# Performance work log

Hardware: AMD Instinct MI355X
Metric: run time of the kernel (lower is better)

Reference implementation:

```python
import jax, jax.numpy as jnp
import numpy as np

D, H, W = 20, 18, 18      # f_dim = (20, 72//4, 72//4); depth == feature_ch
PI = 3.14159              # constant used in the torch module


def make_grid():
    # matches make_coordinate_grid_3d: normalized coords in [-1, 1]
    x = 2.0 * jnp.arange(W, dtype=jnp.float32) / (W - 1) - 1.0
    y = 2.0 * jnp.arange(H, dtype=jnp.float32) / (H - 1) - 1.0
    z = 2.0 * jnp.arange(D, dtype=jnp.float32) / (D - 1) - 1.0
    xx = jnp.broadcast_to(x[None, None, :], (D, H, W))
    yy = jnp.broadcast_to(y[None, :, None], (D, H, W))
    zz = jnp.broadcast_to(z[:, None, None], (D, H, W))
    grid_xy = jnp.stack([xx, yy], axis=-1)   # (D,H,W,2), order (x, y)
    return grid_xy, zz


def trilinear_sample(vol, grid):
    # vol: (D,H,W); grid: (D,H,W,3) with (x,y,z) in [-1,1]
    # F.grid_sample defaults: mode='bilinear' (trilinear), padding='zeros', align_corners=False
    ix = ((grid[..., 0] + 1.0) * W - 1.0) * 0.5
    iy = ((grid[..., 1] + 1.0) * H - 1.0) * 0.5
    iz = ((grid[..., 2] + 1.0) * D - 1.0) * 0.5
    x0, y0, z0 = jnp.floor(ix), jnp.floor(iy), jnp.floor(iz)
    wx, wy, wz = ix - x0, iy - y0, iz - z0
    vflat = vol.reshape(-1)
    out = jnp.zeros_like(ix)
    for cz in (0, 1):
        for cy in (0, 1):
            for cx in (0, 1):
                xi = x0 + cx
                yi = y0 + cy
                zi = z0 + cz
                w = ((wx if cx else 1.0 - wx)
                     * (wy if cy else 1.0 - wy)
                     * (wz if cz else 1.0 - wz))
                valid = ((xi >= 0) & (xi < W) & (yi >= 0) & (yi < H)
                         & (zi >= 0) & (zi < D))
                xi_c = jnp.clip(xi, 0, W - 1).astype(jnp.int32)
                yi_c = jnp.clip(yi, 0, H - 1).astype(jnp.int32)
                zi_c = jnp.clip(zi, 0, D - 1).astype(jnp.int32)
                idx = (zi_c * H + yi_c) * W + xi_c
                out = out + jnp.where(valid, w * vflat[idx], 0.0)
    return out


def setup_inputs() -> dict:
    key = jax.random.key(0)
    ks = jax.random.split(key, 10)
    B, P, F = 4096, 256, 20
    s = 0.05
    return {
        "feature_map": jax.random.normal(ks[0], (B, F, H, W), jnp.float32),
        "para_code": jax.random.normal(ks[1], (B, P), jnp.float32),
        "W1": jax.random.normal(ks[2], (P, P), jnp.float32) * s,
        "b1": jax.random.normal(ks[3], (P,), jnp.float32) * s,
        "Ws": jax.random.normal(ks[4], (P, F), jnp.float32) * s,
        "bs": jax.random.normal(ks[5], (F,), jnp.float32) * s,
        "Wr": jax.random.normal(ks[6], (P, F), jnp.float32) * s,
        "br": jax.random.normal(ks[7], (F,), jnp.float32) * s,
        "Wt": jax.random.normal(ks[8], (P, 2 * F), jnp.float32) * s,
        "bt": jax.random.normal(ks[9], (2 * F,), jnp.float32) * s,
    }


def reference(feature_map, para_code, W1, b1, Ws, bs, Wr, br, Wt, bt):
    B, F = feature_map.shape[0], feature_map.shape[1]  # F == D == 20
    grid_xy, grid_z = make_grid()
    h = jax.nn.relu(para_code @ W1 + b1)                     # commn_linear
    scale = jax.nn.sigmoid(h @ Ws + bs) * 2.0                # (B,F)
    angle = jnp.tanh(h @ Wr + br) * PI                       # (B,F)
    trans = jnp.tanh(h @ Wt + bt).reshape(B, F, 2)           # (B,F,2)
    c, s = jnp.cos(angle), jnp.sin(angle)
    rot = jnp.stack([jnp.stack([c, -s], -1),
                     jnp.stack([s, c], -1)], -2)             # (B,F,2,2)
    g = grid_xy.reshape(F, H * W, 2)                          # depth == feature_ch
    # per-channel affine: rotate, scale, translate each grid point
    tg = jnp.einsum('bfij,fpj->bfpi', rot, g)                 # (B,F,HW,2)
    tg = tg * scale[:, :, None, None] + trans[:, :, None, :]
    full_grid = jnp.concatenate(
        [tg.reshape(B, F, H, W, 2),
         jnp.broadcast_to(grid_z, (B, F, H, W))[..., None]], axis=-1)
    return jax.vmap(trilinear_sample)(feature_map, full_grid)
```

## Files before the change

### kernel.cpp

```cpp
#include <hip/hip_runtime.h>

#define PI_F 3.14159f

__global__ __launch_bounds__(256) void params_kernel(
    const float* __restrict__ pc, const float* __restrict__ W1, const float* __restrict__ b1,
    const float* __restrict__ Ws, const float* __restrict__ bs,
    const float* __restrict__ Wr, const float* __restrict__ br,
    const float* __restrict__ Wt, const float* __restrict__ bt,
    float* __restrict__ params)
{
    __shared__ float hbuf[4][260];
    __shared__ float raw[4][80];

    const int t    = threadIdx.x;
    const int lane = t & 63;
    const int b0   = blockIdx.x * 4;

    float pval[4][4];
    #pragma unroll
    for (int g = 0; g < 4; ++g)
        #pragma unroll
        for (int c = 0; c < 4; ++c)
            pval[g][c] = pc[(size_t)(b0 + g) * 256 + c * 64 + lane];

    float acc[4];
    #pragma unroll
    for (int g = 0; g < 4; ++g) acc[g] = b1[t];

    #pragma unroll
    for (int c = 0; c < 4; ++c) {
        for (int kk = 0; kk < 64; ++kk) {
            float w = W1[(c * 64 + kk) * 256 + t];
            #pragma unroll
            for (int g = 0; g < 4; ++g) {
                float pk = __int_as_float(
                    __builtin_amdgcn_readlane(__float_as_int(pval[g][c]), kk));
                acc[g] = fmaf(pk, w, acc[g]);
            }
        }
    }
    #pragma unroll
    for (int g = 0; g < 4; ++g) hbuf[g][t] = fmaxf(acc[g], 0.0f);
    __syncthreads();

    for (int task = t; task < 320; task += 256) {
        int g   = task / 80;
        int col = task - g * 80;
        const float* Wcol;
        float bias;
        int stride;
        if (col < 20)      { Wcol = Ws + col;        bias = bs[col];      stride = 20; }
        else if (col < 40) { Wcol = Wr + (col - 20); bias = br[col - 20]; stride = 20; }
        else               { Wcol = Wt + (col - 40); bias = bt[col - 40]; stride = 40; }
        const float4* h4 = (const float4*)hbuf[g];
        float a = bias;
        for (int k4 = 0; k4 < 64; ++k4) {
            float4 h = h4[k4];
            int k = k4 * 4;
            a = fmaf(h.x, Wcol[k * stride], a);
            a = fmaf(h.y, Wcol[(k + 1) * stride], a);
            a = fmaf(h.z, Wcol[(k + 2) * stride], a);
            a = fmaf(h.w, Wcol[(k + 3) * stride], a);
        }
        raw[g][col] = a;
    }
    __syncthreads();

    for (int task = t; task < 80; task += 256) {
        int g = task / 20;
        int f = task - g * 20;
        float sc  = 2.0f / (1.0f + expf(-raw[g][f]));
        float ang = PI_F * tanhf(raw[g][20 + f]);
        float tx  = tanhf(raw[g][40 + 2 * f]);
        float ty  = tanhf(raw[g][40 + 2 * f + 1]);
        float c = cosf(ang), s = sinf(ang);
        float* o = params + ((size_t)(b0 + g) * 20 + f) * 8;
        o[0] = 9.0f * sc * c;  o[1] = -9.0f * sc * s;  o[2] = fmaf(9.0f, tx, 9.5f);
        o[3] = 9.0f * sc * s;  o[4] =  9.0f * sc * c;  o[5] = fmaf(9.0f, ty, 9.5f);
        o[6] = 0.0f;           o[7] = 0.0f;
    }
}

template<int D>
struct Stage {
    static constexpr int   Z0  = (D == 0) ? -1 : (40 * D - 19) / 38;
    static constexpr float W1v = (float)((40.0 * D - 19.0) / 38.0 - (double)Z0);
    static constexpr float W0v = 1.0f - W1v;
    static constexpr bool  V0  = (Z0 >= 0);
    static constexpr bool  V1  = (Z0 + 1 <= 19);

    static __device__ __forceinline__ void go(const float (&v)[20], float* vol, int w) {
        float I;
        if constexpr (V0 && V1)  I = fmaf(v[Z0], W0v, v[Z0 + 1] * W1v);
        else if constexpr (V0)   I = v[Z0] * W0v;
        else                     I = v[(Z0 + 1) < 0 ? 0 : (Z0 + 1)] * W1v;
        vol[D * 400 + w] = I;
        Stage<D + 1>::go(v, vol, w);
    }
};
template<> struct Stage<20> {
    static __device__ __forceinline__ void go(const float (&)[20], float*, int) {}
};

__global__ __launch_bounds__(384, 8) void sample_kernel(
    const float* __restrict__ fmap, const float* __restrict__ params,
    float* __restrict__ out)
{
    __shared__ __align__(16) float lds[8192];
    float* vol = lds;
    float* prm = lds + 8024;

    const int b = blockIdx.x;
    const int t = threadIdx.x;

    float4* v4 = (float4*)vol;
    for (int i = t; i < 2006; i += 384) v4[i] = make_float4(0.f, 0.f, 0.f, 0.f);
    if (t < 40)
        ((float4*)prm)[t] = ((const float4*)(params + (size_t)b * 160))[t];
    __syncthreads();

    int yy = 0, xx = 0;
    if (t < 324) {
        yy = t / 18;
        xx = t - yy * 18;
        const float* fb = fmap + (size_t)b * 6480;
        float v[20];
        #pragma unroll
        for (int dz = 0; dz < 20; ++dz) v[dz] = fb[dz * 324 + t];
        const int w = (yy + 1) * 20 + (xx + 1);
        Stage<0>::go(v, vol, w);
    }
    __syncthreads();

    if (t >= 324) return;

    const float X = xx * (2.0f / 17.0f) - 1.0f;
    const float Y = yy * (2.0f / 17.0f) - 1.0f;
    float* ob = out + (size_t)b * 6480 + t;

    #pragma unroll
    for (int G = 0; G < 5; ++G) {
        float u1[4], v1[4];
        int base[4];
        #pragma unroll
        for (int j = 0; j < 4; ++j) {
            const int D = G * 4 + j;
            float4 pA = *(const float4*)(prm + D * 8);
            float2 pB = *(const float2*)(prm + D * 8 + 4);
            float ix = fmaf(pA.x, X, fmaf(pA.y, Y, pA.z));
            float iy = fmaf(pA.w, X, fmaf(pB.x, Y, pB.y));
            ix = fminf(fmaxf(ix, 0.0f), 19.0f);
            iy = fminf(fmaxf(iy, 0.0f), 19.0f);
            float fx = floorf(ix), fy = floorf(iy);
            u1[j] = ix - fx;
            v1[j] = iy - fy;
            base[j] = D * 400 + (int)fy * 20 + (int)fx;
        }
        float t00[4], t01[4], t10[4], t11[4];
        #pragma unroll
        for (int j = 0; j < 4; ++j) {
            const float* s = vol + base[j];
            t00[j] = s[0]; t01[j] = s[1]; t10[j] = s[20]; t11[j] = s[21];
        }
        #pragma unroll
        for (int j = 0; j < 4; ++j) {
            float u0 = 1.0f - u1[j], v0 = 1.0f - v1[j];
            float r = fmaf(fmaf(t01[j], u1[j], t00[j] * u0), v0,
                           fmaf(t11[j], u1[j], t10[j] * u0) * v1[j]);
            ob[(G * 4 + j) * 324] = r;
        }
    }
}

extern "C" void kernel_launch(void* const* d_in, const int* in_sizes, int n_in,
                              void* d_out, int out_size, void* d_ws, size_t ws_size,
                              hipStream_t stream)
{
    const float* fmap = (const float*)d_in[0];
    const float* pc   = (const float*)d_in[1];
    const float* W1   = (const float*)d_in[2];
    const float* b1   = (const float*)d_in[3];
    const float* Ws   = (const float*)d_in[4];
    const float* bs   = (const float*)d_in[5];
    const float* Wr   = (const float*)d_in[6];
    const float* br   = (const float*)d_in[7];
    const float* Wt   = (const float*)d_in[8];
    const float* bt   = (const float*)d_in[9];
    float* out    = (float*)d_out;
    float* params = (float*)d_ws;

    const int B = in_sizes[0] / (20 * 18 * 18);

    params_kernel<<<B / 4, 256, 0, stream>>>(pc, W1, b1, Ws, bs, Wr, br, Wt, bt, params);
    sample_kernel<<<B, 384, 0, stream>>>(fmap, params, out);
}
```

Measured before the change: 243.6 us.

## Split sampling per batch into two 10-channel blocks with border-only LDS zeroing

The sampling kernel now launches two blocks per batch element, each handling 10 of the 20 output channels with a 10-slice z-interpolated volume in LDS. Only the padding border of that volume is zeroed instead of the whole buffer, which removes one barrier. Per-channel affine parameters are now read straight from global memory rather than staged through LDS. The aim is to halve LDS per block for better occupancy, cut zero-fill work and shorten per-block latency. The cost is duplicated index setup and parameter loads across the two halves.

```diff
diff --git a/kernel.cpp b/kernel.cpp
--- a/kernel.cpp
+++ b/kernel.cpp
@@ -81,95 +81,117 @@
     }
 }
 
-template<int D>
+template<int CH0, int J>
 struct Stage {
-    static constexpr int   Z0  = (D == 0) ? -1 : (40 * D - 19) / 38;
-    static constexpr float W1v = (float)((40.0 * D - 19.0) / 38.0 - (double)Z0);
+    static constexpr int   F   = CH0 + J;
+    static constexpr int   Z0g = (F == 0) ? -1 : (40 * F - 19) / 38;
+    static constexpr float W1v = (float)((40.0 * F - 19.0) / 38.0 - (double)Z0g);
     static constexpr float W0v = 1.0f - W1v;
-    static constexpr bool  V0  = (Z0 >= 0);
-    static constexpr bool  V1  = (Z0 + 1 <= 19);
-
-    static __device__ __forceinline__ void go(const float (&v)[20], float* vol, int w) {
+    static constexpr int   S0  = Z0g - CH0;
+    static constexpr bool  V0  = (Z0g >= 0);
+    static constexpr bool  V1  = (Z0g + 1 <= 19);
+
+    static __device__ __forceinline__ void go(const float (&v)[10], float* vol, int w) {
         float I;
-        if constexpr (V0 && V1)  I = fmaf(v[Z0], W0v, v[Z0 + 1] * W1v);
-        else if constexpr (V0)   I = v[Z0] * W0v;
-        else                     I = v[(Z0 + 1) < 0 ? 0 : (Z0 + 1)] * W1v;
-        vol[D * 400 + w] = I;
-        Stage<D + 1>::go(v, vol, w);
+        if constexpr (V0 && V1)  I = fmaf(v[S0], W0v, v[S0 + 1] * W1v);
+        else if constexpr (V0)   I = v[S0] * W0v;
+        else                     I = v[(S0 + 1) < 0 ? 0 : (S0 + 1)] * W1v;
+        vol[J * 400 + w] = I;
+        Stage<CH0, J + 1>::go(v, vol, w);
     }
 };
-template<> struct Stage<20> {
-    static __device__ __forceinline__ void go(const float (&)[20], float*, int) {}
+template<int CH0> struct Stage<CH0, 10> {
+    static __device__ __forceinline__ void go(const float (&)[10], float*, int) {}
 };
+
+template<int CH0>
+__device__ __forceinline__ void sample_half(
+    const float* __restrict__ fmap, const float* __restrict__ params,
+    float* __restrict__ out, int b, int t, float* vol)
+{
+    int yy = 0, xx = 0;
+    float v[10];
+    if (t < 324) {
+        yy = t / 18;
+        xx = t - yy * 18;
+        const float* fb = fmap + (size_t)b * 6480 + CH0 * 324 + t;
+        #pragma unroll
+        for (int k = 0; k < 10; ++k) v[k] = fb[k * 324];
+    }
+
+    float4* v4 = (float4*)vol;
+    for (int i = t; i < 106; i += 384) {
+        int idx;
+        if (i < 100) {
+            int j = i / 10, r = i - j * 10;
+            idx = j * 100 + (r < 5 ? r : 95 + (r - 5));
+        } else {
+            idx = 1000 + (i - 100);
+        }
+        v4[idx] = make_float4(0.f, 0.f, 0.f, 0.f);
+    }
+    for (int i = t; i < 360; i += 384) {
+        int j = i / 36, r = i - j * 36;
+        int y = 1 + (r < 18 ? r : r - 18);
+        int x = (r < 18 ? 0 : 19);
+        vol[j * 400 + y * 20 + x] = 0.0f;
+    }
+
+    if (t < 324) {
+        const int w = (yy + 1) * 20 + (xx + 1);
+        Stage<CH0, 0>::go(v, vol, w);
+    }
+    __syncthreads();
+
+    if (t >= 324) return;
+
+    const float X = xx * (2.0f / 17.0f) - 1.0f;
+    const float Y = yy * (2.0f / 17.0f) - 1.0f;
+    float* ob = out + (size_t)b * 6480 + CH0 * 324 + t;
+    const float* pp = params + ((size_t)b * 20 + CH0) * 8;
+
+    float u1[10], w1_[10];
+    int base[10];
+    #pragma unroll
+    for (int j = 0; j < 10; ++j) {
+        float4 pA = *(const float4*)(pp + j * 8);
+        float2 pB = *(const float2*)(pp + j * 8 + 4);
+        float ix = fmaf(pA.x, X, fmaf(pA.y, Y, pA.z));
+        float iy = fmaf(pA.w, X, fmaf(pB.x, Y, pB.y));
+        ix = fminf(fmaxf(ix, 0.0f), 19.0f);
+        iy = fminf(fmaxf(iy, 0.0f), 19.0f);
+        float fx = floorf(ix), fy = floorf(iy);
+        u1[j]  = ix - fx;
+        w1_[j] = iy - fy;
+        base[j] = j * 400 + (int)fy * 20 + (int)fx;
+    }
+    float t00[10], t01[10], t10[10], t11[10];
+    #pragma unroll
+    for (int j = 0; j < 10; ++j) {
+        const float* s = vol + base[j];
+        t00[j] = s[0]; t01[j] = s[1]; t10[j] = s[20]; t11[j] = s[21];
+    }
+    #pragma unroll
+    for (int j = 0; j < 10; ++j) {
+        float u0 = 1.0f - u1[j], v0 = 1.0f - w1_[j];
+        float r = fmaf(fmaf(t01[j], u1[j], t00[j] * u0), v0,
+                       fmaf(t11[j], u1[j], t10[j] * u0) * w1_[j]);
+        ob[j * 324] = r;
+    }
+}
 
 __global__ __launch_bounds__(384, 8) void sample_kernel(
     const float* __restrict__ fmap, const float* __restrict__ params,
     float* __restrict__ out)
 {
-    __shared__ __align__(16) float lds[8192];
-    float* vol = lds;
-    float* prm = lds + 8024;
-
-    const int b = blockIdx.x;
-    const int t = threadIdx.x;
-
-    float4* v4 = (float4*)vol;
-    for (int i = t; i < 2006; i += 384) v4[i] = make_float4(0.f, 0.f, 0.f, 0.f);
-    if (t < 40)
-        ((float4*)prm)[t] = ((const float4*)(params + (size_t)b * 160))[t];
-    __syncthreads();
-
-    int yy = 0, xx = 0;
-    if (t < 324) {
-        yy = t / 18;
-        xx = t - yy * 18;
-        const float* fb = fmap + (size_t)b * 6480;
-        float v[20];
-        #pragma unroll
-        for (int dz = 0; dz < 20; ++dz) v[dz] = fb[dz * 324 + t];
-        const int w = (yy + 1) * 20 + (xx + 1);
-        Stage<0>::go(v, vol, w);
-    }
-    __syncthreads();
-
-    if (t >= 324) return;
-
-    const float X = xx * (2.0f / 17.0f) - 1.0f;
-    const float Y = yy * (2.0f / 17.0f) - 1.0f;
-    float* ob = out + (size_t)b * 6480 + t;
-
-    #pragma unroll
-    for (int G = 0; G < 5; ++G) {
-        float u1[4], v1[4];
-        int base[4];
-        #pragma unroll
-        for (int j = 0; j < 4; ++j) {
-            const int D = G * 4 + j;
-            float4 pA = *(const float4*)(prm + D * 8);
-            float2 pB = *(const float2*)(prm + D * 8 + 4);
-            float ix = fmaf(pA.x, X, fmaf(pA.y, Y, pA.z));
-            float iy = fmaf(pA.w, X, fmaf(pB.x, Y, pB.y));
-            ix = fminf(fmaxf(ix, 0.0f), 19.0f);
-            iy = fminf(fmaxf(iy, 0.0f), 19.0f);
-            float fx = floorf(ix), fy = floorf(iy);
-            u1[j] = ix - fx;
-            v1[j] = iy - fy;
-            base[j] = D * 400 + (int)fy * 20 + (int)fx;
-        }
-        float t00[4], t01[4], t10[4], t11[4];
-        #pragma unroll
-        for (int j = 0; j < 4; ++j) {
-            const float* s = vol + base[j];
-            t00[j] = s[0]; t01[j] = s[1]; t10[j] = s[20]; t11[j] = s[21];
-        }
-        #pragma unroll
-        for (int j = 0; j < 4; ++j) {
-            float u0 = 1.0f - u1[j], v0 = 1.0f - v1[j];
-            float r = fmaf(fmaf(t01[j], u1[j], t00[j] * u0), v0,
-                           fmaf(t11[j], u1[j], t10[j] * u0) * v1[j]);
-            ob[(G * 4 + j) * 324] = r;
-        }
-    }
+    __shared__ __align__(16) float vol[4024];
+
+    const int bid = blockIdx.x;
+    const int b   = bid >> 1;
+    const int t   = threadIdx.x;
+
+    if (bid & 1) sample_half<10>(fmap, params, out, b, t, vol);
+    else         sample_half<0>(fmap, params, out, b, t, vol);
 }
 
 extern "C" void kernel_launch(void* const* d_in, const int* in_sizes, int n_in,
@@ -192,5 +214,5 @@
     const int B = in_sizes[0] / (20 * 18 * 18);
 
     params_kernel<<<B / 4, 256, 0, stream>>>(pc, W1, b1, Ws, bs, Wr, br, Wt, bt, params);
-    sample_kernel<<<B, 384, 0, stream>>>(fmap, params, out);
-}
+    sample_kernel<<<B * 2, 384, 0, stream>>>(fmap, params, out);
+}
```

Result: no change. 239.5 us (-1.7%).

## Split sampling per output channel across wavefronts with per-slice LDS volumes

Applied to the files above, without the earlier changes.

The sample kernel now assigns each wavefront a single output depth slice instead of having one block build the whole 20x20x20 padded volume in LDS. Each wave blends only its two source z-slices into a 20x20 padded plane and samples from that plane. No block-wide barriers are needed because each wave uses its own LDS region. The grid grows to five blocks per batch item, and each source slice is read about twice from global memory in exchange for much smaller LDS use and higher occupancy.

```diff
diff --git a/kernel.cpp b/kernel.cpp
--- a/kernel.cpp
+++ b/kernel.cpp
@@ -81,93 +81,83 @@
     }
 }
 
-template<int D>
-struct Stage {
-    static constexpr int   Z0  = (D == 0) ? -1 : (40 * D - 19) / 38;
-    static constexpr float W1v = (float)((40.0 * D - 19.0) / 38.0 - (double)Z0);
-    static constexpr float W0v = 1.0f - W1v;
-    static constexpr bool  V0  = (Z0 >= 0);
-    static constexpr bool  V1  = (Z0 + 1 <= 19);
-
-    static __device__ __forceinline__ void go(const float (&v)[20], float* vol, int w) {
-        float I;
-        if constexpr (V0 && V1)  I = fmaf(v[Z0], W0v, v[Z0 + 1] * W1v);
-        else if constexpr (V0)   I = v[Z0] * W0v;
-        else                     I = v[(Z0 + 1) < 0 ? 0 : (Z0 + 1)] * W1v;
-        vol[D * 400 + w] = I;
-        Stage<D + 1>::go(v, vol, w);
-    }
-};
-template<> struct Stage<20> {
-    static __device__ __forceinline__ void go(const float (&)[20], float*, int) {}
-};
-
-__global__ __launch_bounds__(384, 8) void sample_kernel(
+__global__ __launch_bounds__(256, 8) void sample_kernel(
     const float* __restrict__ fmap, const float* __restrict__ params,
     float* __restrict__ out)
 {
-    __shared__ __align__(16) float lds[8192];
-    float* vol = lds;
-    float* prm = lds + 8024;
+    __shared__ __align__(16) float lds[4][424];
 
-    const int b = blockIdx.x;
-    const int t = threadIdx.x;
-
-    float4* v4 = (float4*)vol;
-    for (int i = t; i < 2006; i += 384) v4[i] = make_float4(0.f, 0.f, 0.f, 0.f);
-    if (t < 40)
-        ((float4*)prm)[t] = ((const float4*)(params + (size_t)b * 160))[t];
-    __syncthreads();
-
-    int yy = 0, xx = 0;
-    if (t < 324) {
-        yy = t / 18;
-        xx = t - yy * 18;
-        const float* fb = fmap + (size_t)b * 6480;
-        float v[20];
-        #pragma unroll
-        for (int dz = 0; dz < 20; ++dz) v[dz] = fb[dz * 324 + t];
-        const int w = (yy + 1) * 20 + (xx + 1);
-        Stage<0>::go(v, vol, w);
-    }
-    __syncthreads();
-
-    if (t >= 324) return;
-
-    const float X = xx * (2.0f / 17.0f) - 1.0f;
-    const float Y = yy * (2.0f / 17.0f) - 1.0f;
-    float* ob = out + (size_t)b * 6480 + t;
+    const int t    = threadIdx.x;
+    const int lane = t & 63;
+    const int w    = t >> 6;
+    const int bid  = blockIdx.x;
+    const int b    = bid / 5;
+    const int c    = (bid - b * 5) * 4 + w;
+    float* wv = lds[w];
 
     #pragma unroll
-    for (int G = 0; G < 5; ++G) {
-        float u1[4], v1[4];
-        int base[4];
-        #pragma unroll
-        for (int j = 0; j < 4; ++j) {
-            const int D = G * 4 + j;
-            float4 pA = *(const float4*)(prm + D * 8);
-            float2 pB = *(const float2*)(prm + D * 8 + 4);
+    for (int r = 0; r < 2; ++r) {
+        int i = r * 64 + lane;
+        if (i < 100) {
+            int idx;
+            if (i < 20)      idx = i;
+            else if (i < 40) idx = 380 + (i - 20);
+            else if (i < 76) {
+                int q = i - 40;
+                int y = 1 + (q < 18 ? q : q - 18);
+                idx = y * 20 + (q < 18 ? 0 : 19);
+            } else idx = 400 + (i - 76);
+            wv[idx] = 0.0f;
+        }
+    }
+
+    const float izf = (40.0f * (float)c - 19.0f) * (1.0f / 38.0f);
+    const float fz0 = floorf(izf);
+    const int   z0  = (int)fz0;
+    const float wzB = izf - fz0;
+    const bool  v0  = (z0 >= 0);
+    const bool  v1  = (z0 + 1 <= 19);
+    const float ew0 = v0 ? (1.0f - wzB) : 0.0f;
+    const float ew1 = v1 ? wzB : 0.0f;
+    const float* fb = fmap + (size_t)b * 6480;
+    const float* s0 = fb + (v0 ? z0 : 0) * 324;
+    const float* s1 = fb + (v1 ? z0 + 1 : 19) * 324;
+
+    #pragma unroll
+    for (int it = 0; it < 6; ++it) {
+        int i = it * 64 + lane;
+        if (i < 324) {
+            float a  = s0[i];
+            float bb = s1[i];
+            int y = i / 18, x = i - y * 18;
+            wv[(y + 1) * 20 + (x + 1)] = fmaf(a, ew0, bb * ew1);
+        }
+    }
+
+    const float* pp = params + ((size_t)b * 20 + c) * 8;
+    const float4 pA = *(const float4*)pp;
+    const float2 pB = *(const float2*)(pp + 4);
+
+    float* ob = out + (size_t)b * 6480 + c * 324;
+    #pragma unroll
+    for (int it = 0; it < 6; ++it) {
+        int i = it * 64 + lane;
+        if (i < 324) {
+            int y = i / 18, x = i - y * 18;
+            float X = (float)x * (2.0f / 17.0f) - 1.0f;
+            float Y = (float)y * (2.0f / 17.0f) - 1.0f;
             float ix = fmaf(pA.x, X, fmaf(pA.y, Y, pA.z));
             float iy = fmaf(pA.w, X, fmaf(pB.x, Y, pB.y));
             ix = fminf(fmaxf(ix, 0.0f), 19.0f);
             iy = fminf(fmaxf(iy, 0.0f), 19.0f);
             float fx = floorf(ix), fy = floorf(iy);
-            u1[j] = ix - fx;
-            v1[j] = iy - fy;
-            base[j] = D * 400 + (int)fy * 20 + (int)fx;
-        }
-        float t00[4], t01[4], t10[4], t11[4];
-        #pragma unroll
-        for (int j = 0; j < 4; ++j) {
-            const float* s = vol + base[j];
-            t00[j] = s[0]; t01[j] = s[1]; t10[j] = s[20]; t11[j] = s[21];
-        }
-        #pragma unroll
-        for (int j = 0; j < 4; ++j) {
-            float u0 = 1.0f - u1[j], v0 = 1.0f - v1[j];
-            float r = fmaf(fmaf(t01[j], u1[j], t00[j] * u0), v0,
-                           fmaf(t11[j], u1[j], t10[j] * u0) * v1[j]);
-            ob[(G * 4 + j) * 324] = r;
+            float u1 = ix - fx, vv = iy - fy;
+            const float* s = wv + ((int)fy * 20 + (int)fx);
+            float t00 = s[0], t01 = s[1], t10 = s[20], t11 = s[21];
+            float u0 = 1.0f - u1, vc = 1.0f - vv;
+            float r = fmaf(fmaf(t01, u1, t00 * u0), vc,
+                           fmaf(t11, u1, t10 * u0) * vv);
+            ob[i] = r;
         }
     }
 }
@@ -192,5 +182,5 @@
     const int B = in_sizes[0] / (20 * 18 * 18);
 
     params_kernel<<<B / 4, 256, 0, stream>>>(pc, W1, b1, Ws, bs, Wr, br, Wt, bt, params);
-    sample_kernel<<<B, 384, 0, stream>>>(fmap, params, out);
+    sample_kernel<<<B * 5, 256, 0, stream>>>(fmap, params, out);
 }
```

Result: no change. 242.6 us (-0.4%).
